# Performance work log

Measured on AMD Instinct MI355X. Metric: run time of the kernel, lower is better.

Reference implementation:

```python
import jax, jax.numpy as jnp
import numpy as np
import math

NHEAD = 8
OUT = 64
EF = 64
IN = 256
NTYPES = 5
NH = 50000
NT = 100000
E = 800000
NEG_SLOPE = 0.2

def _uniform(key, shape, fan):
    # matches reset(): uniform(-stdv, stdv), stdv = sqrt(6/(fan_in+fan_out)) over last two dims
    stdv = math.sqrt(6.0 / (shape[-2] + shape[-1]))
    return jax.random.uniform(key, shape, jnp.float32, -stdv, stdv)

def setup_inputs() -> dict:
    key = jax.random.key(0)
    ks = jax.random.split(key, 12)
    head_feature = jax.random.normal(ks[0], (NH, IN), jnp.float32)
    tail_feature = jax.random.normal(ks[1], (NT, IN), jnp.float32)
    head_ind = jax.random.randint(ks[2], (E,), 0, NH)
    tail_ind = jax.random.randint(ks[3], (E,), 0, NT)
    tmp_edge = jax.random.randint(ks[4], (E,), 0, NTYPES)
    edge_emb = _uniform(ks[5], (NTYPES, EF), None)
    W = _uniform(ks[6], (IN, OUT * NHEAD), None)
    W_e = _uniform(ks[7], (EF, EF * NHEAD), None)
    a_l = _uniform(ks[8], (1, NHEAD, OUT), None)
    a_r = _uniform(ks[9], (1, NHEAD, OUT), None)
    a_e = _uniform(ks[10], (1, NHEAD, EF), None)
    return {"head_feature": head_feature, "tail_feature": tail_feature,
            "head_ind": head_ind, "tail_ind": tail_ind, "tmp_edge": tmp_edge,
            "edge_emb": edge_emb, "W": W, "W_e": W_e,
            "a_l": a_l, "a_r": a_r, "a_e": a_e}

def reference(head_feature, tail_feature, head_ind, tail_ind, tmp_edge,
              edge_emb, W, W_e, a_l, a_r, a_e):
    n_head_nodes = head_feature.shape[0]
    # projections (dropout is identity in eval)
    h_head = (head_feature @ W).reshape(-1, NHEAD, OUT)   # [NH, H, D]
    h_tail = (tail_feature @ W).reshape(-1, NHEAD, OUT)   # [NT, H, D]
    e = (edge_emb @ W_e).reshape(-1, NHEAD, EF)           # [T, H, EF]
    # per-edge attention logits, all heads at once: [E, H]
    h_l = jnp.sum(a_l * h_head, axis=-1)[head_ind]
    h_r = jnp.sum(a_r * h_tail, axis=-1)[tail_ind]
    h_e = jnp.sum(a_e * e, axis=-1)[tmp_edge]
    att = jax.nn.leaky_relu(h_l + h_r + h_e, NEG_SLOPE)
    # sparse (per-destination-row) softmax, vectorized over heads
    seg_max = jax.ops.segment_max(att, head_ind, num_segments=n_head_nodes)
    att = jnp.exp(att - seg_max[head_ind])
    denom = jax.ops.segment_sum(att, head_ind, num_segments=n_head_nodes)
    att = att / denom[head_ind]                           # [E, H]
    # weighted aggregation per head (small fixed loop over heads)
    outs = [jax.ops.segment_sum(att[:, n:n + 1] * h_tail[tail_ind, n, :],
                                head_ind, num_segments=n_head_nodes)
            for n in range(NHEAD)]
    out = jnp.stack(outs, axis=1).reshape(n_head_nodes, -1)  # [NH, H*D]
    return out, att
```

## Files before the change

kernel.cpp:

```cpp
#include <hip/hip_runtime.h>

#define NH 50000
#define NT 100000
#define NE 800000
#define MPAD 100096

typedef __attribute__((ext_vector_type(8))) short bf16x8;
typedef __attribute__((ext_vector_type(4))) float f32x4;
typedef __attribute__((ext_vector_type(8))) unsigned short u16x8;
typedef __attribute__((ext_vector_type(4))) unsigned int u32x4;

__device__ __forceinline__ unsigned short f2bf(float f){
  unsigned int u = __float_as_uint(f);
  u += 0x7FFFu + ((u >> 16) & 1u);
  return (unsigned short)(u >> 16);
}

__device__ __forceinline__ void fma8(float* acc, float w, uint4 pk){
  acc[0] += w*__uint_as_float(pk.x<<16); acc[1] += w*__uint_as_float(pk.x&0xFFFF0000u);
  acc[2] += w*__uint_as_float(pk.y<<16); acc[3] += w*__uint_as_float(pk.y&0xFFFF0000u);
  acc[4] += w*__uint_as_float(pk.z<<16); acc[5] += w*__uint_as_float(pk.z&0xFFFF0000u);
  acc[6] += w*__uint_as_float(pk.w<<16); acc[7] += w*__uint_as_float(pk.w&0xFFFF0000u);
}

__device__ __forceinline__ void gl2lds16(const unsigned short* g, unsigned short* l){
  __builtin_amdgcn_global_load_lds(
      (const __attribute__((address_space(1))) void*)g,
      (__attribute__((address_space(3))) void*)l, 16, 0, 0);
}

__global__ __launch_bounds__(256) void k_fuse1(
      const float* __restrict__ tail_f, unsigned short* __restrict__ A_bf,
      const int* __restrict__ head_ind, int* __restrict__ cnt,
      const float* __restrict__ W, unsigned short* __restrict__ Wt,
      const float* __restrict__ W_e, const float* __restrict__ edge_emb,
      const float* __restrict__ a_l, const float* __restrict__ a_r,
      const float* __restrict__ a_e,
      unsigned short* __restrict__ wlr_t, float* __restrict__ h_e){
  __shared__ float s_al[512], s_ar[512], s_ae[512], s_wef[512];
  int b = blockIdx.x, t = threadIdx.x;
  if (b < 12500){
    size_t g = (size_t)b*256 + t;
    const float* src = tail_f + g*8;
    float4 v0 = *(const float4*)(src);
    float4 v1 = *(const float4*)(src + 4);
    u16x8 s;
    s[0]=f2bf(v0.x); s[1]=f2bf(v0.y); s[2]=f2bf(v0.z); s[3]=f2bf(v0.w);
    s[4]=f2bf(v1.x); s[5]=f2bf(v1.y); s[6]=f2bf(v1.z); s[7]=f2bf(v1.w);
    *(u16x8*)(A_bf + g*8) = s;
  } else if (b < 15625){
    int e = (b-12500)*256 + t;
    atomicAdd(&cnt[head_ind[e]], 1);
  } else if (b < 16137){
    int n = b - 15625, k = t;
    Wt[n*256+k] = f2bf(W[k*512+n]);
  } else {
    for (int i=t;i<512;i+=256){ s_al[i]=a_l[i]; s_ar[i]=a_r[i]; s_ae[i]=a_e[i]; }
    __syncthreads();
    { int k = t;
      for (int h=0;h<8;h++){
        float accl=0.f, accr=0.f;
        for (int d=0; d<64; d++){
          float w = W[k*512 + h*64 + d];
          accl += w*s_al[h*64+d];
          accr += w*s_ar[h*64+d];
        }
        wlr_t[h*256 + k]     = f2bf(accl);
        wlr_t[(8+h)*256 + k] = f2bf(accr);
      }
    }
    if (t<64){
      for (int h=0;h<8;h++){
        float acc=0.f;
        for (int f=0; f<64; f++) acc += W_e[t*512 + h*64 + f]*s_ae[h*64+f];
        s_wef[t*8+h]=acc;
      }
    }
    __syncthreads();
    if (t<40){
      int ty=t>>3, h=t&7;
      float acc=0.f;
      for (int k2=0;k2<64;k2++) acc += edge_emb[ty*64+k2]*s_wef[k2*8+h];
      h_e[t]=acc;
    }
  }
}

__device__ __forceinline__ void gemm3_body(unsigned short* smem, int bid,
      const unsigned short* __restrict__ A_bf, const unsigned short* __restrict__ Wt,
      const float* __restrict__ a_r_g, unsigned short* __restrict__ Cout,
      float* __restrict__ h_r){
  unsigned short* As0 = smem;
  unsigned short* As1 = smem + 8192;
  int t = threadIdx.x;
  int wave = t>>6, lane = t&63;
  int lr = lane & 15, lq = lane >> 4;

  int wg  = (bid & 7)*391 + (bid >> 3);
  int m0 = (wg >> 2)*128;
  int n0 = (wg & 3)*128;
  int wm = (wave>>1)*64, wn = (wave&1)*64;

  f32x4 acc[4][4];
#pragma unroll
  for (int mf=0;mf<4;mf++)
#pragma unroll
    for (int nf=0;nf<4;nf++) acc[mf][nf] = (f32x4){0.f,0.f,0.f,0.f};

  bf16x8 b0[8], b1[8], b2[8], b3[8];

#define STAGEA(dst, kt) do { \
    _Pragma("unroll") \
    for (int i=0;i<4;i++){ \
      int v = wave*256 + i*64 + lane; \
      int row = v>>3, un = (v&7) ^ (row&7); \
      gl2lds16(A_bf + (size_t)(m0+row)*256 + (kt)*64 + un*8, \
               &(dst)[(wave*256 + i*64)*8]); \
    } } while(0)

#define LOADB(kt, bb) do { \
    _Pragma("unroll") \
    for (int ks=0;ks<2;ks++) \
      _Pragma("unroll") \
      for (int nf=0;nf<4;nf++){ \
        int c = wn + nf*16 + lr; \
        (bb)[ks*4+nf] = *(const bf16x8*)(Wt + (size_t)(n0+c)*256 + ((kt)*8+ks*4+lq)*8); \
      } } while(0)

#define COMPUTE(Asb, bb) do { \
    _Pragma("unroll") \
    for (int ks=0;ks<2;ks++){ \
      bf16x8 af[4]; \
      _Pragma("unroll") \
      for (int mf=0;mf<4;mf++){ \
        int r = wm + mf*16 + lr; \
        int u = (ks*4 + lq) ^ (r&7); \
        af[mf] = *(const bf16x8*)((const char*)(Asb) + r*128 + u*16); \
      } \
      _Pragma("unroll") \
      for (int mf=0;mf<4;mf++) \
        _Pragma("unroll") \
        for (int nf=0;nf<4;nf++) \
          acc[mf][nf] = __builtin_amdgcn_mfma_f32_16x16x32_bf16(af[mf], (bb)[ks*4+nf], acc[mf][nf], 0,0,0); \
    } } while(0)

#define WAITV(N) asm volatile("s_waitcnt vmcnt(" #N ")" ::: "memory")
#define RBAR() do { __builtin_amdgcn_s_barrier(); __builtin_amdgcn_sched_barrier(0); } while(0)

  STAGEA(As0, 0); LOADB(0, b0);
  STAGEA(As1, 1); LOADB(1, b1);
  WAITV(20); RBAR();
  COMPUTE(As0, b0);
  RBAR();
  STAGEA(As0, 2); LOADB(2, b2);
  WAITV(20); RBAR();
  COMPUTE(As1, b1);
  RBAR();
  STAGEA(As1, 3); LOADB(3, b3);
  WAITV(20); RBAR();
  COMPUTE(As0, b2);
  WAITV(8);  RBAR();
  COMPUTE(As1, b3);
#undef STAGEA
#undef LOADB
#undef COMPUTE
#undef WAITV
#undef RBAR

  {
    int h = (n0 + wn) >> 6;
    float w[4];
#pragma unroll
    for (int nf=0;nf<4;nf++) w[nf] = a_r_g[h*64 + nf*16 + lr];
#pragma unroll
    for (int mf=0;mf<4;mf++)
#pragma unroll
      for (int j=0;j<4;j++){
        float s = acc[mf][0][j]*w[0] + acc[mf][1][j]*w[1]
                + acc[mf][2][j]*w[2] + acc[mf][3][j]*w[3];
        s += __shfl_xor(s, 1); s += __shfl_xor(s, 2);
        s += __shfl_xor(s, 4); s += __shfl_xor(s, 8);
        int gr = m0 + wm + mf*16 + lq*4 + j;
        if (lr == 0 && gr < NT) h_r[(size_t)gr*8 + h] = s;
      }
  }

  __syncthreads();
  unsigned short* Cs = smem;
#pragma unroll
  for (int mf=0;mf<4;mf++)
#pragma unroll
    for (int nf=0;nf<4;nf++)
#pragma unroll
      for (int j=0;j<4;j++){
        int row = wm + mf*16 + lq*4 + j;
        int cb  = (wn + nf*16 + lr)*2;
        *(unsigned short*)((char*)Cs + row*256 + (cb ^ ((row&12)<<3))) = f2bf(acc[mf][nf][j]);
      }
  __syncthreads();
#pragma unroll
  for (int i=0;i<8;i++){
    int v = i*256 + t;
    int row = v>>4, u = v&15;
    u32x4 val = *(const u32x4*)((const char*)Cs + row*256 + ((u*16) ^ ((row&12)<<3)));
    *(u32x4*)(Cout + (size_t)(m0+row)*512 + n0 + u*8) = val;
  }
}

__device__ __forceinline__ void hl_body(unsigned short* As, unsigned short* Bs, int bid,
      const float* __restrict__ head_f, const unsigned short* __restrict__ wlr_t,
      float* __restrict__ h_l){
  int t = threadIdx.x;
  int wave = t>>6, lane = t&63;
  int lr = lane&15, lq = lane>>4;
  long r0 = (long)bid*256;

#pragma unroll
  for (int i=0;i<2;i++){
    int q = i*256 + t;
    int c = q>>5, un = q&31;
    float4 v = *(const float4*)(wlr_t + c*256 + un*8);
    int u = un ^ (c&7);
    *(float4*)((char*)Bs + c*512 + u*16) = v;
  }

  f32x4 acc[4];
#pragma unroll
  for (int mf=0;mf<4;mf++) acc[mf]=(f32x4){0.f,0.f,0.f,0.f};

  for (int kt=0; kt<4; kt++){
    __syncthreads();
#pragma unroll
    for (int i=0;i<16;i++){
      int q = i*256+t;
      int row = q>>4, cg = q&15;
      long gr = r0 + row;
      float4 v = make_float4(0.f,0.f,0.f,0.f);
      if (gr < NH) v = *(const float4*)(head_f + gr*256 + kt*64 + cg*4);
      int u = (cg>>1) ^ (row&7);
      ushort4 sv;
      sv.x=f2bf(v.x); sv.y=f2bf(v.y); sv.z=f2bf(v.z); sv.w=f2bf(v.w);
      *(ushort4*)((char*)As + row*128 + u*16 + (cg&1)*8) = sv;
    }
    __syncthreads();
#pragma unroll
    for (int ks=0;ks<2;ks++){
      int un = kt*8 + ks*4 + lq;
      int cu = un ^ (lr&7);
      bf16x8 bfr = *(const bf16x8*)((const char*)Bs + lr*512 + cu*16);
#pragma unroll
      for (int mf=0;mf<4;mf++){
        int r = wave*64 + mf*16 + lr;
        int u = (ks*4+lq) ^ (r&7);
        bf16x8 afr = *(const bf16x8*)((const char*)As + r*128 + u*16);
        acc[mf] = __builtin_amdgcn_mfma_f32_16x16x32_bf16(afr, bfr, acc[mf], 0,0,0);
      }
    }
  }
#pragma unroll
  for (int mf=0;mf<4;mf++)
#pragma unroll
    for (int j=0;j<4;j++){
      long grow = r0 + wave*64 + mf*16 + lq*4 + j;
      if (grow < NH && lr < 8) h_l[grow*8+lr] = acc[mf][j];
    }
}

__global__ __launch_bounds__(256) void k_fuse2(
      const unsigned short* __restrict__ A_bf, const unsigned short* __restrict__ Wt,
      const float* __restrict__ a_r_g, unsigned short* __restrict__ Cout,
      float* __restrict__ h_r,
      const float* __restrict__ head_f, const unsigned short* __restrict__ wlr_t,
      float* __restrict__ h_l){
  __shared__ __align__(16) unsigned short smem[20480];
  if (blockIdx.x < 3128)
    gemm3_body(smem, blockIdx.x, A_bf, Wt, a_r_g, Cout, h_r);
  else
    hl_body(smem, smem + 16384, blockIdx.x - 3128, head_f, wlr_t, h_l);
}

__global__ void k_scan1(const int* __restrict__ cnt, int* __restrict__ bsum){
  __shared__ int s[256];
  int b=blockIdx.x, t=threadIdx.x, g=b*256+t;
  s[t] = (g<NH)? cnt[g] : 0;
  __syncthreads();
  for (int off=128; off>0; off>>=1){ if (t<off) s[t]+=s[t+off]; __syncthreads(); }
  if (t==0) bsum[b]=s[0];
}
__global__ void k_scan3(const int* __restrict__ cnt, const int* __restrict__ bsum,
                        int* __restrict__ offs, int* __restrict__ cur){
  __shared__ int s[256];
  __shared__ int sb[196];
  int b=blockIdx.x, t=threadIdx.x, g=b*256+t;
  if (t < 196) sb[t] = bsum[t];
  int v=(g<NH)? cnt[g] : 0;
  s[t]=v; __syncthreads();
  for (int off=1; off<256; off<<=1){
    int u=(t>=off)? s[t-off] : 0; __syncthreads();
    s[t]+=u; __syncthreads();
  }
  int base = 0;
  for (int j=0;j<b;j++) base += sb[j];
  int excl = s[t]-v + base;
  if (g<NH){
    offs[g]=excl; cur[g]=excl;
    if (g==NH-1) offs[NH]=excl+v;
  }
}

__global__ void k_logit2(const int* __restrict__ head_ind, const int* __restrict__ tail_ind,
                         const int* __restrict__ tmp_edge,
                         const float* __restrict__ h_l, const float* __restrict__ h_r,
                         const float* __restrict__ h_e,
                         int* __restrict__ cur,
                         float* __restrict__ att_csr,
                         int* __restrict__ edge_of, int* __restrict__ tail_s){
  int g = blockIdx.x*256 + threadIdx.x;
  int e = g>>3, h = g&7, l = threadIdx.x&63;
  int hd = head_ind[e], tl = tail_ind[e], ty = tmp_edge[e];
  float v = h_l[hd*8+h] + h_r[(size_t)tl*8+h] + h_e[ty*8+h];
  v = v > 0.f ? v : 0.2f*v;
  int p = 0;
  if (h==0) p = atomicAdd(&cur[hd], 1);
  p = __shfl(p, l & ~7);
  att_csr[p*8+h] = v;
  if (h==0){ edge_of[p]=e; tail_s[p]=tl; }
}

__global__ __launch_bounds__(256) void k_agg3(const int* __restrict__ offs,
      const int* __restrict__ edge_of, const int* __restrict__ tail_s,
      const float* __restrict__ att_csr,
      const unsigned short* __restrict__ h_tail,
      float* __restrict__ att, float* __restrict__ out){
  int t = threadIdx.x;
  int l = t & 63;
  int i = blockIdx.x*4 + (t>>6);
  int h = l & 7, hq = l >> 3;
  int s0 = offs[i];
  int deg = offs[i+1] - s0;

  float m = -1e30f;
  for (int q = hq; q < deg; q += 8) m = fmaxf(m, att_csr[(s0+q)*8 + h]);
  m = fmaxf(m, __shfl_xor(m, 8));
  m = fmaxf(m, __shfl_xor(m, 16));
  m = fmaxf(m, __shfl_xor(m, 32));
  float sum = 0.f;
  for (int q = hq; q < deg; q += 8) sum += __expf(att_csr[(s0+q)*8 + h] - m);
  sum += __shfl_xor(sum, 8); sum += __shfl_xor(sum, 16); sum += __shfl_xor(sum, 32);
  float r = (deg > 0) ? 1.f/sum : 0.f;

  float mh = __shfl(m, hq), rh = __shfl(r, hq);
  bool wlane = (l & 7) == 0;
  float acc[8];
#pragma unroll
  for (int c=0;c<8;c++) acc[c]=0.f;
  int j = 0;
  for (; j+4 <= deg; j += 4){
    int p0=s0+j, p1=p0+1, p2=p0+2, p3=p0+3;
    int t0=tail_s[p0], t1=tail_s[p1], t2=tail_s[p2], t3=tail_s[p3];
    float a0=att_csr[p0*8+hq], a1=att_csr[p1*8+hq];
    float a2=att_csr[p2*8+hq], a3=att_csr[p3*8+hq];
    uint4 r0 = *(const uint4*)(h_tail + (size_t)t0*512 + l*8);
    uint4 r1 = *(const uint4*)(h_tail + (size_t)t1*512 + l*8);
    uint4 r2 = *(const uint4*)(h_tail + (size_t)t2*512 + l*8);
    uint4 r3 = *(const uint4*)(h_tail + (size_t)t3*512 + l*8);
    float w0=__expf(a0-mh)*rh, w1=__expf(a1-mh)*rh;
    float w2=__expf(a2-mh)*rh, w3=__expf(a3-mh)*rh;
    if (wlane){
      __builtin_nontemporal_store(w0, &att[(size_t)edge_of[p0]*8 + hq]);
      __builtin_nontemporal_store(w1, &att[(size_t)edge_of[p1]*8 + hq]);
      __builtin_nontemporal_store(w2, &att[(size_t)edge_of[p2]*8 + hq]);
      __builtin_nontemporal_store(w3, &att[(size_t)edge_of[p3]*8 + hq]);
    }
    fma8(acc, w0, r0);
    fma8(acc, w1, r1);
    fma8(acc, w2, r2);
    fma8(acc, w3, r3);
  }
  for (; j < deg; j++){
    int p0 = s0+j;
    int t0 = tail_s[p0];
    float a0 = att_csr[p0*8 + hq];
    uint4 r0 = *(const uint4*)(h_tail + (size_t)t0*512 + l*8);
    float w0 = __expf(a0 - mh) * rh;
    if (wlane) __builtin_nontemporal_store(w0, &att[(size_t)edge_of[p0]*8 + hq]);
    fma8(acc, w0, r0);
  }
  float* o = out + (size_t)i*512 + l*8;
  f32x4 v0 = {acc[0],acc[1],acc[2],acc[3]};
  f32x4 v1 = {acc[4],acc[5],acc[6],acc[7]};
  __builtin_nontemporal_store(v0, (f32x4*)o);
  __builtin_nontemporal_store(v1, (f32x4*)(o+4));
}

extern "C" void kernel_launch(void* const* d_in, const int* in_sizes, int n_in,
                              void* d_out, int out_size, void* d_ws, size_t ws_size,
                              hipStream_t stream) {
  const float* head_f   = (const float*)d_in[0];
  const float* tail_f   = (const float*)d_in[1];
  const int*   head_ind = (const int*)d_in[2];
  const int*   tail_ind = (const int*)d_in[3];
  const int*   tmp_edge = (const int*)d_in[4];
  const float* edge_emb = (const float*)d_in[5];
  const float* W        = (const float*)d_in[6];
  const float* W_e      = (const float*)d_in[7];
  const float* a_l      = (const float*)d_in[8];
  const float* a_r      = (const float*)d_in[9];
  const float* a_e      = (const float*)d_in[10];

  float* out = (float*)d_out;
  float* att = out + (size_t)NH*512;
  unsigned short* A_bf = (unsigned short*)d_out;

  char* ws = (char*)d_ws;
  auto alloc = [&](size_t bytes)->char*{ char* p = ws; ws += (bytes+511)&~(size_t)511; return p; };
  unsigned short* Wt    = (unsigned short*)alloc((size_t)512*256*2);
  unsigned short* wlr_t = (unsigned short*)alloc((size_t)16*256*2);
  float* h_e            = (float*)alloc(512);
  float* h_l            = (float*)alloc((size_t)NH*8*4);
  float* h_r            = (float*)alloc((size_t)NT*8*4);
  unsigned short* h_tail= (unsigned short*)alloc((size_t)MPAD*512*2);
  int* cnt              = (int*)alloc((size_t)NH*4);
  int* offs             = (int*)alloc((size_t)(NH+1)*4);
  int* cur              = (int*)alloc((size_t)NH*4);
  int* bsum             = (int*)alloc(1024);
  int* edge_of          = (int*)alloc((size_t)NE*4);
  int* tail_s           = (int*)alloc((size_t)NE*4);
  float* att_csr        = (float*)alloc((size_t)NE*8*4);

  hipMemsetAsync(cnt, 0, (size_t)NH*4, stream);
  k_fuse1<<<16138,256,0,stream>>>(tail_f, A_bf, head_ind, cnt, W, Wt,
                                  W_e, edge_emb, a_l, a_r, a_e, wlr_t, h_e);
  k_fuse2<<<3128+196,256,0,stream>>>(A_bf, Wt, a_r, h_tail, h_r, head_f, wlr_t, h_l);
  k_scan1<<<196,256,0,stream>>>(cnt, bsum);
  k_scan3<<<196,256,0,stream>>>(cnt, bsum, offs, cur);
  k_logit2<<<NE*8/256,256,0,stream>>>(head_ind, tail_ind, tmp_edge, h_l, h_r, h_e,
                                      cur, att_csr, edge_of, tail_s);
  k_agg3<<<NH/4,256,0,stream>>>(offs, edge_of, tail_s, att_csr, h_tail, att, out);
}
```

Measured before the change: 418.2 us.

## Fold scan into GEMM launch and use persistent atomic work queue in aggregation

Replaces the two-kernel prefix scan with a single-block scan run as block 0 of the fused GEMM kernel, removing two launches and their serialization. The aggregation kernel becomes persistent (2048 blocks) with waves pulling destination rows from a global atomic counter, aiming to balance uneven row degrees and cut block scheduling overhead. The single-block scan is serial (196 elements per thread) and may land on the critical path. The atomic per row adds contention.

After: 1.043 ms. 2.49x slower.

```diff
diff --git a/kernel.cpp b/kernel.cpp
--- a/kernel.cpp
+++ b/kernel.cpp
@@ -86,6 +86,26 @@
   }
 }
 
+__device__ __forceinline__ void scan_body(int* s,
+      const int* __restrict__ cnt, int* __restrict__ offs, int* __restrict__ cur){
+  int t = threadIdx.x;
+  int base_i = t*196;
+  int sum = 0;
+  for (int j=0;j<196;j++){ int g=base_i+j; sum += (g<NH)? cnt[g] : 0; }
+  s[t] = sum; __syncthreads();
+  int v = sum;
+  for (int off=1; off<256; off<<=1){
+    int u = (t>=off)? s[t-off] : 0; __syncthreads();
+    s[t] += u; __syncthreads();
+  }
+  int run = s[t] - v;
+  for (int j=0;j<196;j++){
+    int g = base_i + j;
+    if (g < NH){ int c = cnt[g]; offs[g]=run; cur[g]=run; run += c; }
+  }
+  if (t==255) offs[NH] = s[t];
+}
+
 __device__ __forceinline__ void gemm3_body(unsigned short* smem, int bid,
       const unsigned short* __restrict__ A_bf, const unsigned short* __restrict__ Wt,
       const float* __restrict__ a_r_g, unsigned short* __restrict__ Cout,
@@ -271,41 +291,15 @@
       const float* __restrict__ a_r_g, unsigned short* __restrict__ Cout,
       float* __restrict__ h_r,
       const float* __restrict__ head_f, const unsigned short* __restrict__ wlr_t,
-      float* __restrict__ h_l){
+      float* __restrict__ h_l,
+      const int* __restrict__ cnt, int* __restrict__ offs, int* __restrict__ cur){
   __shared__ __align__(16) unsigned short smem[20480];
-  if (blockIdx.x < 3128)
-    gemm3_body(smem, blockIdx.x, A_bf, Wt, a_r_g, Cout, h_r);
+  if (blockIdx.x == 0)
+    scan_body((int*)smem, cnt, offs, cur);
+  else if (blockIdx.x <= 3128)
+    gemm3_body(smem, blockIdx.x - 1, A_bf, Wt, a_r_g, Cout, h_r);
   else
-    hl_body(smem, smem + 16384, blockIdx.x - 3128, head_f, wlr_t, h_l);
-}
-
-__global__ void k_scan1(const int* __restrict__ cnt, int* __restrict__ bsum){
-  __shared__ int s[256];
-  int b=blockIdx.x, t=threadIdx.x, g=b*256+t;
-  s[t] = (g<NH)? cnt[g] : 0;
-  __syncthreads();
-  for (int off=128; off>0; off>>=1){ if (t<off) s[t]+=s[t+off]; __syncthreads(); }
-  if (t==0) bsum[b]=s[0];
-}
-__global__ void k_scan3(const int* __restrict__ cnt, const int* __restrict__ bsum,
-                        int* __restrict__ offs, int* __restrict__ cur){
-  __shared__ int s[256];
-  __shared__ int sb[196];
-  int b=blockIdx.x, t=threadIdx.x, g=b*256+t;
-  if (t < 196) sb[t] = bsum[t];
-  int v=(g<NH)? cnt[g] : 0;
-  s[t]=v; __syncthreads();
-  for (int off=1; off<256; off<<=1){
-    int u=(t>=off)? s[t-off] : 0; __syncthreads();
-    s[t]+=u; __syncthreads();
-  }
-  int base = 0;
-  for (int j=0;j<b;j++) base += sb[j];
-  int excl = s[t]-v + base;
-  if (g<NH){
-    offs[g]=excl; cur[g]=excl;
-    if (g==NH-1) offs[NH]=excl+v;
-  }
+    hl_body(smem, smem + 16384, blockIdx.x - 3129, head_f, wlr_t, h_l);
 }
 
 __global__ void k_logit2(const int* __restrict__ head_ind, const int* __restrict__ tail_ind,
@@ -327,70 +321,78 @@
   if (h==0){ edge_of[p]=e; tail_s[p]=tl; }
 }
 
-__global__ __launch_bounds__(256) void k_agg3(const int* __restrict__ offs,
+__global__ __launch_bounds__(256) void k_agg4(const int* __restrict__ offs,
       const int* __restrict__ edge_of, const int* __restrict__ tail_s,
       const float* __restrict__ att_csr,
       const unsigned short* __restrict__ h_tail,
+      int* __restrict__ wctr,
       float* __restrict__ att, float* __restrict__ out){
   int t = threadIdx.x;
   int l = t & 63;
-  int i = blockIdx.x*4 + (t>>6);
   int h = l & 7, hq = l >> 3;
-  int s0 = offs[i];
-  int deg = offs[i+1] - s0;
-
-  float m = -1e30f;
-  for (int q = hq; q < deg; q += 8) m = fmaxf(m, att_csr[(s0+q)*8 + h]);
-  m = fmaxf(m, __shfl_xor(m, 8));
-  m = fmaxf(m, __shfl_xor(m, 16));
-  m = fmaxf(m, __shfl_xor(m, 32));
-  float sum = 0.f;
-  for (int q = hq; q < deg; q += 8) sum += __expf(att_csr[(s0+q)*8 + h] - m);
-  sum += __shfl_xor(sum, 8); sum += __shfl_xor(sum, 16); sum += __shfl_xor(sum, 32);
-  float r = (deg > 0) ? 1.f/sum : 0.f;
-
-  float mh = __shfl(m, hq), rh = __shfl(r, hq);
-  bool wlane = (l & 7) == 0;
-  float acc[8];
-#pragma unroll
-  for (int c=0;c<8;c++) acc[c]=0.f;
-  int j = 0;
-  for (; j+4 <= deg; j += 4){
-    int p0=s0+j, p1=p0+1, p2=p0+2, p3=p0+3;
-    int t0=tail_s[p0], t1=tail_s[p1], t2=tail_s[p2], t3=tail_s[p3];
-    float a0=att_csr[p0*8+hq], a1=att_csr[p1*8+hq];
-    float a2=att_csr[p2*8+hq], a3=att_csr[p3*8+hq];
-    uint4 r0 = *(const uint4*)(h_tail + (size_t)t0*512 + l*8);
-    uint4 r1 = *(const uint4*)(h_tail + (size_t)t1*512 + l*8);
-    uint4 r2 = *(const uint4*)(h_tail + (size_t)t2*512 + l*8);
-    uint4 r3 = *(const uint4*)(h_tail + (size_t)t3*512 + l*8);
-    float w0=__expf(a0-mh)*rh, w1=__expf(a1-mh)*rh;
-    float w2=__expf(a2-mh)*rh, w3=__expf(a3-mh)*rh;
-    if (wlane){
-      __builtin_nontemporal_store(w0, &att[(size_t)edge_of[p0]*8 + hq]);
-      __builtin_nontemporal_store(w1, &att[(size_t)edge_of[p1]*8 + hq]);
-      __builtin_nontemporal_store(w2, &att[(size_t)edge_of[p2]*8 + hq]);
-      __builtin_nontemporal_store(w3, &att[(size_t)edge_of[p3]*8 + hq]);
-    }
-    fma8(acc, w0, r0);
-    fma8(acc, w1, r1);
-    fma8(acc, w2, r2);
-    fma8(acc, w3, r3);
-  }
-  for (; j < deg; j++){
-    int p0 = s0+j;
-    int t0 = tail_s[p0];
-    float a0 = att_csr[p0*8 + hq];
-    uint4 r0 = *(const uint4*)(h_tail + (size_t)t0*512 + l*8);
-    float w0 = __expf(a0 - mh) * rh;
-    if (wlane) __builtin_nontemporal_store(w0, &att[(size_t)edge_of[p0]*8 + hq]);
-    fma8(acc, w0, r0);
-  }
-  float* o = out + (size_t)i*512 + l*8;
-  f32x4 v0 = {acc[0],acc[1],acc[2],acc[3]};
-  f32x4 v1 = {acc[4],acc[5],acc[6],acc[7]};
-  __builtin_nontemporal_store(v0, (f32x4*)o);
-  __builtin_nontemporal_store(v1, (f32x4*)(o+4));
+
+  while (true){
+    int i;
+    if (l == 0) i = atomicAdd(wctr, 1);
+    i = __shfl(i, 0);
+    if (i >= NH) break;
+
+    int s0 = offs[i];
+    int deg = offs[i+1] - s0;
+
+    float m = -1e30f;
+    for (int q = hq; q < deg; q += 8) m = fmaxf(m, att_csr[(s0+q)*8 + h]);
+    m = fmaxf(m, __shfl_xor(m, 8));
+    m = fmaxf(m, __shfl_xor(m, 16));
+    m = fmaxf(m, __shfl_xor(m, 32));
+    float sum = 0.f;
+    for (int q = hq; q < deg; q += 8) sum += __expf(att_csr[(s0+q)*8 + h] - m);
+    sum += __shfl_xor(sum, 8); sum += __shfl_xor(sum, 16); sum += __shfl_xor(sum, 32);
+    float r = (deg > 0) ? 1.f/sum : 0.f;
+
+    float mh = __shfl(m, hq), rh = __shfl(r, hq);
+    bool wlane = (l & 7) == 0;
+    float acc[8];
+#pragma unroll
+    for (int c=0;c<8;c++) acc[c]=0.f;
+    int j = 0;
+    for (; j+4 <= deg; j += 4){
+      int p0=s0+j, p1=p0+1, p2=p0+2, p3=p0+3;
+      int t0=tail_s[p0], t1=tail_s[p1], t2=tail_s[p2], t3=tail_s[p3];
+      float a0=att_csr[p0*8+hq], a1=att_csr[p1*8+hq];
+      float a2=att_csr[p2*8+hq], a3=att_csr[p3*8+hq];
+      uint4 r0 = *(const uint4*)(h_tail + (size_t)t0*512 + l*8);
+      uint4 r1 = *(const uint4*)(h_tail + (size_t)t1*512 + l*8);
+      uint4 r2 = *(const uint4*)(h_tail + (size_t)t2*512 + l*8);
+      uint4 r3 = *(const uint4*)(h_tail + (size_t)t3*512 + l*8);
+      float w0=__expf(a0-mh)*rh, w1=__expf(a1-mh)*rh;
+      float w2=__expf(a2-mh)*rh, w3=__expf(a3-mh)*rh;
+      if (wlane){
+        __builtin_nontemporal_store(w0, &att[(size_t)edge_of[p0]*8 + hq]);
+        __builtin_nontemporal_store(w1, &att[(size_t)edge_of[p1]*8 + hq]);
+        __builtin_nontemporal_store(w2, &att[(size_t)edge_of[p2]*8 + hq]);
+        __builtin_nontemporal_store(w3, &att[(size_t)edge_of[p3]*8 + hq]);
+      }
+      fma8(acc, w0, r0);
+      fma8(acc, w1, r1);
+      fma8(acc, w2, r2);
+      fma8(acc, w3, r3);
+    }
+    for (; j < deg; j++){
+      int p0 = s0+j;
+      int t0 = tail_s[p0];
+      float a0 = att_csr[p0*8 + hq];
+      uint4 r0 = *(const uint4*)(h_tail + (size_t)t0*512 + l*8);
+      float w0 = __expf(a0 - mh) * rh;
+      if (wlane) __builtin_nontemporal_store(w0, &att[(size_t)edge_of[p0]*8 + hq]);
+      fma8(acc, w0, r0);
+    }
+    float* o = out + (size_t)i*512 + l*8;
+    f32x4 v0 = {acc[0],acc[1],acc[2],acc[3]};
+    f32x4 v1 = {acc[4],acc[5],acc[6],acc[7]};
+    __builtin_nontemporal_store(v0, (f32x4*)o);
+    __builtin_nontemporal_store(v1, (f32x4*)(o+4));
+  }
 }
 
 extern "C" void kernel_launch(void* const* d_in, const int* in_sizes, int n_in,
@@ -420,21 +422,20 @@
   float* h_l            = (float*)alloc((size_t)NH*8*4);
   float* h_r            = (float*)alloc((size_t)NT*8*4);
   unsigned short* h_tail= (unsigned short*)alloc((size_t)MPAD*512*2);
-  int* cnt              = (int*)alloc((size_t)NH*4);
+  int* cnt              = (int*)alloc((size_t)(NH+1)*4);
   int* offs             = (int*)alloc((size_t)(NH+1)*4);
   int* cur              = (int*)alloc((size_t)NH*4);
-  int* bsum             = (int*)alloc(1024);
   int* edge_of          = (int*)alloc((size_t)NE*4);
   int* tail_s           = (int*)alloc((size_t)NE*4);
   float* att_csr        = (float*)alloc((size_t)NE*8*4);
-
-  hipMemsetAsync(cnt, 0, (size_t)NH*4, stream);
+  int* wctr             = cnt + NH;
+
+  hipMemsetAsync(cnt, 0, (size_t)(NH+1)*4, stream);
   k_fuse1<<<16138,256,0,stream>>>(tail_f, A_bf, head_ind, cnt, W, Wt,
                                   W_e, edge_emb, a_l, a_r, a_e, wlr_t, h_e);
-  k_fuse2<<<3128+196,256,0,stream>>>(A_bf, Wt, a_r, h_tail, h_r, head_f, wlr_t, h_l);
-  k_scan1<<<196,256,0,stream>>>(cnt, bsum);
-  k_scan3<<<196,256,0,stream>>>(cnt, bsum, offs, cur);
+  k_fuse2<<<1+3128+196,256,0,stream>>>(A_bf, Wt, a_r, h_tail, h_r,
+                                       head_f, wlr_t, h_l, cnt, offs, cur);
   k_logit2<<<NE*8/256,256,0,stream>>>(head_ind, tail_ind, tmp_edge, h_l, h_r, h_e,
                                       cur, att_csr, edge_of, tail_s);
-  k_agg3<<<NH/4,256,0,stream>>>(offs, edge_of, tail_s, att_csr, h_tail, att, out);
-}
+  k_agg4<<<2048,256,0,stream>>>(offs, edge_of, tail_s, att_csr, h_tail, wctr, att, out);
+}
```
